# Performance work log

Hardware: AMD Instinct MI355X
Metric: run time of the kernel (lower is better)

Reference implementation:

```python
import jax, jax.numpy as jnp
import numpy as np

NODE_NUM = 20000
NUM_CENTROIDS = 64
EMBED_SIZE = 128
EPS = 1e-5
POINT_SCALE = 0.1 / np.sqrt(EMBED_SIZE)  # keep Poincare-ball norms << 1


def setup_inputs() -> dict:
    key = jax.random.key(0)
    k1, k2 = jax.random.split(key)
    node_repr = jax.random.normal(k1, (NODE_NUM, EMBED_SIZE), dtype=jnp.float32) * POINT_SCALE
    centroid_weight = jax.random.normal(k2, (NUM_CENTROIDS, EMBED_SIZE), dtype=jnp.float32) * POINT_SCALE
    mask = jnp.ones((NODE_NUM, 1), dtype=jnp.float32)
    return {"node_repr": node_repr, "mask": mask, "centroid_weight": centroid_weight}


def _poincare_pairwise_dist(u, v):
    # u: [N, E], v: [C, E] -> [N, C]
    # d(u,v) = arccosh(1 + 2*||u-v||^2 / ((1-||u||^2)(1-||v||^2)))
    su = jnp.sum(u * u, axis=-1)                      # [N]
    sv = jnp.sum(v * v, axis=-1)                      # [C]
    dot = jnp.einsum('ne,ce->nc', u, v)               # [N, C]
    sqdist = su[:, None] + sv[None, :] - 2.0 * dot    # ||u-v||^2, [N, C]
    sqdist = jnp.maximum(sqdist, 0.0)
    denom = jnp.maximum((1.0 - su)[:, None] * (1.0 - sv)[None, :], EPS)
    arg = jnp.maximum(1.0 + 2.0 * sqdist / denom, 1.0 + EPS)
    return jnp.arccosh(arg)


def reference(node_repr, mask, centroid_weight):
    node_num = node_repr.shape[0]
    num_centroids = centroid_weight.shape[0]
    # fused pairwise manifold distance, no [N*C, E] materialization
    dist = _poincare_pairwise_dist(node_repr, centroid_weight)      # [N, C]
    node_centroid_dist = dist[None, :, :] * mask[None, :, :]        # [1, N, C] (mask broadcasts [N,1])
    graph_centroid_dist = jnp.sum(node_centroid_dist, axis=1) / jnp.sum(mask)  # [1, C]
    return (graph_centroid_dist, node_centroid_dist)
```

## Files before the change

kernel.cpp:

```cpp
#include <hip/hip_runtime.h>
#include <hip/hip_bf16.h>
#include <math.h>

#define EMBED  128
#define NUM_C  64
#define EPS    1e-5f
#define NPB    32
#define LDSROW 132

typedef __attribute__((ext_vector_type(8))) short bf16x8;
typedef __attribute__((ext_vector_type(4))) float f32x4;

__device__ __forceinline__ bf16x8 pack8(float4 x, float4 y) {
    __hip_bfloat162 p0 = __float22bfloat162_rn(float2{x.x, x.y});
    __hip_bfloat162 p1 = __float22bfloat162_rn(float2{x.z, x.w});
    __hip_bfloat162 p2 = __float22bfloat162_rn(float2{y.x, y.y});
    __hip_bfloat162 p3 = __float22bfloat162_rn(float2{y.z, y.w});
    union { __hip_bfloat162 h[4]; bf16x8 v; } u;
    u.h[0] = p0; u.h[1] = p1; u.h[2] = p2; u.h[3] = p3;
    return u.v;
}

__global__ __launch_bounds__(256) void cd_main(
    const float* __restrict__ node_repr,
    const float* __restrict__ mask,
    const float* __restrict__ cent,
    float* __restrict__ out,
    float* __restrict__ wcol,
    float* __restrict__ wmsk,
    int N, int nb, int atomicMode)
{
    __shared__ float sa[NPB * LDSROW];
    __shared__ float s_su[NPB];
    __shared__ float s_ms[NPB];

    const int tid  = threadIdx.x;
    const int lane = tid & 63;
    const int wv   = tid >> 6;
    const int quad = lane >> 4;
    const int lm   = lane & 15;
    const int cw   = wv * 16;
    const int node0 = blockIdx.x * NPB;

    const int srow = tid >> 3;
    const int scol = (tid & 7) * 16;
    {
        int row = node0 + srow;
        int rc  = row < N ? row : N - 1;
        const float* p = node_repr + (long)rc * EMBED + scol;
        float4 r0 = *(const float4*)(p);
        float4 r1 = *(const float4*)(p + 4);
        float4 r2 = *(const float4*)(p + 8);
        float4 r3 = *(const float4*)(p + 12);
        float mrow = (row < N) ? mask[rc] : 0.f;

        float* dst = &sa[srow * LDSROW + scol];
        *(float4*)(dst)      = r0;
        *(float4*)(dst + 4)  = r1;
        *(float4*)(dst + 8)  = r2;
        *(float4*)(dst + 12) = r3;

        float pp = 0.f;
        pp = fmaf(r0.x,r0.x, fmaf(r0.y,r0.y, fmaf(r0.z,r0.z, fmaf(r0.w,r0.w, pp))));
        pp = fmaf(r1.x,r1.x, fmaf(r1.y,r1.y, fmaf(r1.z,r1.z, fmaf(r1.w,r1.w, pp))));
        pp = fmaf(r2.x,r2.x, fmaf(r2.y,r2.y, fmaf(r2.z,r2.z, fmaf(r2.w,r2.w, pp))));
        pp = fmaf(r3.x,r3.x, fmaf(r3.y,r3.y, fmaf(r3.z,r3.z, fmaf(r3.w,r3.w, pp))));
        pp += __shfl_xor(pp, 1); pp += __shfl_xor(pp, 2); pp += __shfl_xor(pp, 4);
        if ((tid & 7) == 0) { s_su[srow] = pp; s_ms[srow] = mrow; }
    }

    const float* bp = cent + (long)(cw + lm) * EMBED + quad * 8;
    float svp = 0.f;
    bf16x8 bb[4];
    #pragma unroll
    for (int ks = 0; ks < 4; ++ks) {
        float4 b0 = *(const float4*)(bp + ks * 32);
        float4 b1 = *(const float4*)(bp + ks * 32 + 4);
        svp = fmaf(b0.x,b0.x, fmaf(b0.y,b0.y, fmaf(b0.z,b0.z, fmaf(b0.w,b0.w, svp))));
        svp = fmaf(b1.x,b1.x, fmaf(b1.y,b1.y, fmaf(b1.z,b1.z, fmaf(b1.w,b1.w, svp))));
        bb[ks] = pack8(b0, b1);
    }
    svp += __shfl_xor(svp, 16); svp += __shfl_xor(svp, 32);
    const float sv1 = 1.f - svp;

    __syncthreads();

    f32x4 acc0 = {0.f,0.f,0.f,0.f}, acc1 = {0.f,0.f,0.f,0.f};
    #pragma unroll
    for (int ks = 0; ks < 4; ++ks) {
        const int base = quad * 8 + ks * 32;
        float4 a00 = *(const float4*)&sa[lm * LDSROW + base];
        float4 a01 = *(const float4*)&sa[lm * LDSROW + base + 4];
        float4 a10 = *(const float4*)&sa[(16 + lm) * LDSROW + base];
        float4 a11 = *(const float4*)&sa[(16 + lm) * LDSROW + base + 4];
        acc0 = __builtin_amdgcn_mfma_f32_16x16x32_bf16(pack8(a00, a01), bb[ks], acc0, 0, 0, 0);
        acc1 = __builtin_amdgcn_mfma_f32_16x16x32_bf16(pack8(a10, a11), bb[ks], acc1, 0, 0, 0);
    }

    float gcol = 0.f;
    #pragma unroll
    for (int r = 0; r < 4; ++r) {
        const int m0 = quad * 4 + r;
        {
            const int n = node0 + m0;
            const float su_m = s_su[m0];
            const float mk_m = s_ms[m0];
            float sq    = fmaxf(su_m + svp - 2.f * acc0[r], 0.f);
            float denom = fmaxf((1.f - su_m) * sv1, EPS);
            float tt    = fmaxf(2.f * sq * __builtin_amdgcn_rcpf(denom), EPS);
            float v     = __logf(1.f + tt + sqrtf(tt * (tt + 2.f))) * mk_m;
            if (n < N) { out[NUM_C + (long)n * NUM_C + cw + lm] = v; gcol += v; }
        }
        {
            const int n = node0 + 16 + m0;
            const float su_m = s_su[16 + m0];
            const float mk_m = s_ms[16 + m0];
            float sq    = fmaxf(su_m + svp - 2.f * acc1[r], 0.f);
            float denom = fmaxf((1.f - su_m) * sv1, EPS);
            float tt    = fmaxf(2.f * sq * __builtin_amdgcn_rcpf(denom), EPS);
            float v     = __logf(1.f + tt + sqrtf(tt * (tt + 2.f))) * mk_m;
            if (n < N) { out[NUM_C + (long)n * NUM_C + cw + lm] = v; gcol += v; }
        }
    }

    gcol += __shfl_xor(gcol, 16); gcol += __shfl_xor(gcol, 32);
    if (quad == 0) {
        if (atomicMode) atomicAdd(&wcol[cw + lm], gcol);
        else            wcol[(long)(cw + lm) * nb + blockIdx.x] = gcol;
    }
    if (wv == 0) {
        float ms = (lane < NPB) ? s_ms[lane] : 0.f;
        #pragma unroll
        for (int k = 32; k; k >>= 1) ms += __shfl_xor(ms, k, 64);
        if (lane == 0) {
            if (atomicMode) atomicAdd(&wmsk[0], ms);
            else            wmsk[blockIdx.x] = ms;
        }
    }
}

__global__ __launch_bounds__(256) void cd_fin1(
    const float* __restrict__ wcol, const float* __restrict__ wmsk,
    float* __restrict__ out, int nb)
{
    __shared__ float rs[4], rm[4];
    const int c   = blockIdx.x;
    const int tid = threadIdx.x;

    float s = 0.f, m = 0.f;
    for (int b = tid; b < nb; b += 256) {
        s += wcol[(long)c * nb + b];
        m += wmsk[b];
    }
    #pragma unroll
    for (int k = 32; k; k >>= 1) { s += __shfl_xor(s, k, 64); m += __shfl_xor(m, k, 64); }
    if ((tid & 63) == 0) { rs[tid >> 6] = s; rm[tid >> 6] = m; }
    __syncthreads();
    if (tid == 0)
        out[c] = (rs[0] + rs[1] + rs[2] + rs[3]) / (rm[0] + rm[1] + rm[2] + rm[3]);
}

__global__ void cd_zero(float* acc) { if (threadIdx.x < NUM_C + 1) acc[threadIdx.x] = 0.f; }
__global__ void cd_fin_atomic(const float* __restrict__ acc, float* __restrict__ out) {
    int c = threadIdx.x;
    if (c < NUM_C) out[c] = acc[c] / acc[NUM_C];
}

extern "C" void kernel_launch(void* const* d_in, const int* in_sizes, int n_in,
                              void* d_out, int out_size, void* d_ws, size_t ws_size,
                              hipStream_t stream) {
    const float* node_repr = (const float*)d_in[0];
    const float* mask      = (const float*)d_in[1];
    const float* cent      = (const float*)d_in[2];
    float* out = (float*)d_out;

    const int N  = in_sizes[0] / EMBED;
    const int nb = (N + NPB - 1) / NPB;
    const size_t needed = ((size_t)NUM_C * nb + nb) * sizeof(float);

    if (ws_size >= needed) {
        float* wcol = (float*)d_ws;
        float* wmsk = wcol + (size_t)NUM_C * nb;
        cd_main<<<nb, 256, 0, stream>>>(node_repr, mask, cent, out, wcol, wmsk, N, nb, 0);
        cd_fin1<<<NUM_C, 256, 0, stream>>>(wcol, wmsk, out, nb);
    } else {
        float* acc = (float*)d_ws;
        cd_zero<<<1, 128, 0, stream>>>(acc);
        cd_main<<<nb, 256, 0, stream>>>(node_repr, mask, cent, out, acc, acc + NUM_C, N, nb, 1);
        cd_fin_atomic<<<1, 64, 0, stream>>>(acc, out);
    }
}
```

Before: 71.55 us.

## Swap MFMA operands to drop LDS staging and vectorize output stores

Centroids become the A operand and node rows are loaded straight from global memory into registers as the B operand. This removes the LDS tile, the __syncthreads and the shared row norms and mask. With the transposed accumulator layout, each lane holds four consecutive centroids for one node, so the output can be written as float4 instead of scalar stores. Column sums now need 16-lane shuffle reductions. Each of the four waves reloads the same 32 node rows from global memory instead of sharing them through LDS.

Measured after the change: 74.30 us. +3.8%, slower.

```diff
diff --git a/kernel.cpp b/kernel.cpp
--- a/kernel.cpp
+++ b/kernel.cpp
@@ -6,7 +6,6 @@
 #define NUM_C  64
 #define EPS    1e-5f
 #define NPB    32
-#define LDSROW 132
 
 typedef __attribute__((ext_vector_type(8))) short bf16x8;
 typedef __attribute__((ext_vector_type(4))) float f32x4;
@@ -30,10 +29,6 @@
     float* __restrict__ wmsk,
     int N, int nb, int atomicMode)
 {
-    __shared__ float sa[NPB * LDSROW];
-    __shared__ float s_su[NPB];
-    __shared__ float s_ms[NPB];
-
     const int tid  = threadIdx.x;
     const int lane = tid & 63;
     const int wv   = tid >> 6;
@@ -42,96 +37,107 @@
     const int cw   = wv * 16;
     const int node0 = blockIdx.x * NPB;
 
-    const int srow = tid >> 3;
-    const int scol = (tid & 7) * 16;
-    {
-        int row = node0 + srow;
-        int rc  = row < N ? row : N - 1;
-        const float* p = node_repr + (long)rc * EMBED + scol;
-        float4 r0 = *(const float4*)(p);
-        float4 r1 = *(const float4*)(p + 4);
-        float4 r2 = *(const float4*)(p + 8);
-        float4 r3 = *(const float4*)(p + 12);
-        float mrow = (row < N) ? mask[rc] : 0.f;
-
-        float* dst = &sa[srow * LDSROW + scol];
-        *(float4*)(dst)      = r0;
-        *(float4*)(dst + 4)  = r1;
-        *(float4*)(dst + 8)  = r2;
-        *(float4*)(dst + 12) = r3;
-
-        float pp = 0.f;
-        pp = fmaf(r0.x,r0.x, fmaf(r0.y,r0.y, fmaf(r0.z,r0.z, fmaf(r0.w,r0.w, pp))));
-        pp = fmaf(r1.x,r1.x, fmaf(r1.y,r1.y, fmaf(r1.z,r1.z, fmaf(r1.w,r1.w, pp))));
-        pp = fmaf(r2.x,r2.x, fmaf(r2.y,r2.y, fmaf(r2.z,r2.z, fmaf(r2.w,r2.w, pp))));
-        pp = fmaf(r3.x,r3.x, fmaf(r3.y,r3.y, fmaf(r3.z,r3.z, fmaf(r3.w,r3.w, pp))));
-        pp += __shfl_xor(pp, 1); pp += __shfl_xor(pp, 2); pp += __shfl_xor(pp, 4);
-        if ((tid & 7) == 0) { s_su[srow] = pp; s_ms[srow] = mrow; }
+    const float* ap = cent + (long)(cw + lm) * EMBED + quad * 8;
+    float svp = 0.f;
+    bf16x8 aa[4];
+    #pragma unroll
+    for (int ks = 0; ks < 4; ++ks) {
+        float4 a0 = *(const float4*)(ap + ks * 32);
+        float4 a1 = *(const float4*)(ap + ks * 32 + 4);
+        svp = fmaf(a0.x,a0.x, fmaf(a0.y,a0.y, fmaf(a0.z,a0.z, fmaf(a0.w,a0.w, svp))));
+        svp = fmaf(a1.x,a1.x, fmaf(a1.y,a1.y, fmaf(a1.z,a1.z, fmaf(a1.w,a1.w, svp))));
+        aa[ks] = pack8(a0, a1);
+    }
+    svp += __shfl_xor(svp, 16); svp += __shfl_xor(svp, 32);
+    float svr[4], sv1r[4];
+    #pragma unroll
+    for (int r = 0; r < 4; ++r) {
+        svr[r]  = __shfl(svp, quad * 4 + r);
+        sv1r[r] = 1.f - svr[r];
     }
 
-    const float* bp = cent + (long)(cw + lm) * EMBED + quad * 8;
-    float svp = 0.f;
-    bf16x8 bb[4];
+    const int n0 = node0 + lm;
+    const int n1 = node0 + 16 + lm;
+    const int c0 = (n0 < N) ? n0 : N - 1;
+    const int c1 = (n1 < N) ? n1 : N - 1;
+    const float* p0 = node_repr + (long)c0 * EMBED + quad * 8;
+    const float* p1 = node_repr + (long)c1 * EMBED + quad * 8;
+    float su0 = 0.f, su1 = 0.f;
+    bf16x8 b0[4], b1[4];
     #pragma unroll
     for (int ks = 0; ks < 4; ++ks) {
-        float4 b0 = *(const float4*)(bp + ks * 32);
-        float4 b1 = *(const float4*)(bp + ks * 32 + 4);
-        svp = fmaf(b0.x,b0.x, fmaf(b0.y,b0.y, fmaf(b0.z,b0.z, fmaf(b0.w,b0.w, svp))));
-        svp = fmaf(b1.x,b1.x, fmaf(b1.y,b1.y, fmaf(b1.z,b1.z, fmaf(b1.w,b1.w, svp))));
-        bb[ks] = pack8(b0, b1);
+        float4 x0 = *(const float4*)(p0 + ks * 32);
+        float4 x1 = *(const float4*)(p0 + ks * 32 + 4);
+        float4 y0 = *(const float4*)(p1 + ks * 32);
+        float4 y1 = *(const float4*)(p1 + ks * 32 + 4);
+        su0 = fmaf(x0.x,x0.x, fmaf(x0.y,x0.y, fmaf(x0.z,x0.z, fmaf(x0.w,x0.w, su0))));
+        su0 = fmaf(x1.x,x1.x, fmaf(x1.y,x1.y, fmaf(x1.z,x1.z, fmaf(x1.w,x1.w, su0))));
+        su1 = fmaf(y0.x,y0.x, fmaf(y0.y,y0.y, fmaf(y0.z,y0.z, fmaf(y0.w,y0.w, su1))));
+        su1 = fmaf(y1.x,y1.x, fmaf(y1.y,y1.y, fmaf(y1.z,y1.z, fmaf(y1.w,y1.w, su1))));
+        b0[ks] = pack8(x0, x1);
+        b1[ks] = pack8(y0, y1);
     }
-    svp += __shfl_xor(svp, 16); svp += __shfl_xor(svp, 32);
-    const float sv1 = 1.f - svp;
-
-    __syncthreads();
+    su0 += __shfl_xor(su0, 16); su0 += __shfl_xor(su0, 32);
+    su1 += __shfl_xor(su1, 16); su1 += __shfl_xor(su1, 32);
+    const float mk0 = (n0 < N) ? mask[c0] : 0.f;
+    const float mk1 = (n1 < N) ? mask[c1] : 0.f;
 
     f32x4 acc0 = {0.f,0.f,0.f,0.f}, acc1 = {0.f,0.f,0.f,0.f};
     #pragma unroll
     for (int ks = 0; ks < 4; ++ks) {
-        const int base = quad * 8 + ks * 32;
-        float4 a00 = *(const float4*)&sa[lm * LDSROW + base];
-        float4 a01 = *(const float4*)&sa[lm * LDSROW + base + 4];
-        float4 a10 = *(const float4*)&sa[(16 + lm) * LDSROW + base];
-        float4 a11 = *(const float4*)&sa[(16 + lm) * LDSROW + base + 4];
-        acc0 = __builtin_amdgcn_mfma_f32_16x16x32_bf16(pack8(a00, a01), bb[ks], acc0, 0, 0, 0);
-        acc1 = __builtin_amdgcn_mfma_f32_16x16x32_bf16(pack8(a10, a11), bb[ks], acc1, 0, 0, 0);
+        acc0 = __builtin_amdgcn_mfma_f32_16x16x32_bf16(aa[ks], b0[ks], acc0, 0, 0, 0);
+        acc1 = __builtin_amdgcn_mfma_f32_16x16x32_bf16(aa[ks], b1[ks], acc1, 0, 0, 0);
     }
 
-    float gcol = 0.f;
+    const float o0 = 1.f - su0, o1 = 1.f - su1;
+    float v0a[4], v1a[4], g[4];
     #pragma unroll
     for (int r = 0; r < 4; ++r) {
-        const int m0 = quad * 4 + r;
         {
-            const int n = node0 + m0;
-            const float su_m = s_su[m0];
-            const float mk_m = s_ms[m0];
-            float sq    = fmaxf(su_m + svp - 2.f * acc0[r], 0.f);
-            float denom = fmaxf((1.f - su_m) * sv1, EPS);
-            float tt    = fmaxf(2.f * sq * __builtin_amdgcn_rcpf(denom), EPS);
-            float v     = __logf(1.f + tt + sqrtf(tt * (tt + 2.f))) * mk_m;
-            if (n < N) { out[NUM_C + (long)n * NUM_C + cw + lm] = v; gcol += v; }
+            float sq = fmaxf(su0 + svr[r] - 2.f * acc0[r], 0.f);
+            float dn = fmaxf(o0 * sv1r[r], EPS);
+            float tt = fmaxf(2.f * sq * __builtin_amdgcn_rcpf(dn), EPS);
+            v0a[r] = __logf(1.f + tt + sqrtf(tt * (tt + 2.f))) * mk0;
         }
         {
-            const int n = node0 + 16 + m0;
-            const float su_m = s_su[16 + m0];
-            const float mk_m = s_ms[16 + m0];
-            float sq    = fmaxf(su_m + svp - 2.f * acc1[r], 0.f);
-            float denom = fmaxf((1.f - su_m) * sv1, EPS);
-            float tt    = fmaxf(2.f * sq * __builtin_amdgcn_rcpf(denom), EPS);
-            float v     = __logf(1.f + tt + sqrtf(tt * (tt + 2.f))) * mk_m;
-            if (n < N) { out[NUM_C + (long)n * NUM_C + cw + lm] = v; gcol += v; }
+            float sq = fmaxf(su1 + svr[r] - 2.f * acc1[r], 0.f);
+            float dn = fmaxf(o1 * sv1r[r], EPS);
+            float tt = fmaxf(2.f * sq * __builtin_amdgcn_rcpf(dn), EPS);
+            v1a[r] = __logf(1.f + tt + sqrtf(tt * (tt + 2.f))) * mk1;
+        }
+        g[r] = v0a[r] + v1a[r];
+    }
+    if (n0 < N) {
+        float4 V0 = {v0a[0], v0a[1], v0a[2], v0a[3]};
+        *(float4*)(out + NUM_C + (long)n0 * NUM_C + cw + quad * 4) = V0;
+    }
+    if (n1 < N) {
+        float4 V1 = {v1a[0], v1a[1], v1a[2], v1a[3]};
+        *(float4*)(out + NUM_C + (long)n1 * NUM_C + cw + quad * 4) = V1;
+    }
+
+    #pragma unroll
+    for (int r = 0; r < 4; ++r) {
+        g[r] += __shfl_xor(g[r], 1);
+        g[r] += __shfl_xor(g[r], 2);
+        g[r] += __shfl_xor(g[r], 4);
+        g[r] += __shfl_xor(g[r], 8);
+    }
+    if (lm == 0) {
+        if (atomicMode) {
+            #pragma unroll
+            for (int r = 0; r < 4; ++r) atomicAdd(&wcol[cw + quad * 4 + r], g[r]);
+        } else {
+            #pragma unroll
+            for (int r = 0; r < 4; ++r)
+                wcol[(long)(cw + quad * 4 + r) * nb + blockIdx.x] = g[r];
         }
     }
 
-    gcol += __shfl_xor(gcol, 16); gcol += __shfl_xor(gcol, 32);
-    if (quad == 0) {
-        if (atomicMode) atomicAdd(&wcol[cw + lm], gcol);
-        else            wcol[(long)(cw + lm) * nb + blockIdx.x] = gcol;
-    }
     if (wv == 0) {
-        float ms = (lane < NPB) ? s_ms[lane] : 0.f;
-        #pragma unroll
-        for (int k = 32; k; k >>= 1) ms += __shfl_xor(ms, k, 64);
+        float ms = mk0 + mk1;
+        ms += __shfl_xor(ms, 1); ms += __shfl_xor(ms, 2);
+        ms += __shfl_xor(ms, 4); ms += __shfl_xor(ms, 8);
         if (lane == 0) {
             if (atomicMode) atomicAdd(&wmsk[0], ms);
             else            wmsk[blockIdx.x] = ms;
```
